# Kernel optimization log

Hardware: AMD Instinct MI355X
Metric: run time of the kernel (lower is better)

## Reference

```python
import jax, jax.numpy as jnp
import numpy as np

B, T, D = 4, 2048, 128

def setup_inputs() -> dict:
    key = jax.random.key(0)
    k1, k2, k3 = jax.random.split(key, 3)
    x = jax.random.normal(k1, (B, T, D), dtype=jnp.float32)
    # torch nn.Linear default init ~ U(-1/sqrt(D), 1/sqrt(D))
    lim = 1.0 / np.sqrt(D)
    W = jax.random.uniform(k2, (3 * D, D), dtype=jnp.float32, minval=-lim, maxval=lim)
    b = jax.random.uniform(k3, (3 * D,), dtype=jnp.float32, minval=-lim, maxval=lim)
    return {"x": x, "W": W, "b": b}

def reference(x, W, b):
    Bx, Tx, Dx = x.shape
    qkv = (x @ W.T + b).reshape(Bx, Tx, 3, Dx)
    q, k, v = qkv[:, :, 0], qkv[:, :, 1], qkv[:, :, 2]
    # positive feature map: elu(x) + 1
    q = jax.nn.elu(q) + 1.0
    k = jax.nn.elu(k) + 1.0
    # causal linear attention via outer-product cumsum (same math as torch module)
    kv = jnp.einsum('bti,btj->btij', k, v)      # (B,T,D,D)
    kv_cum = jnp.cumsum(kv, axis=1)             # prefix sums of k v^T
    k_cum = jnp.cumsum(k, axis=1)               # prefix sums of k
    num = jnp.einsum('bti,btij->btj', q, kv_cum)
    den = jnp.einsum('bti,bti->bt', q, k_cum)[..., None] + 1e-6
    return num / den
```

## Files before the change

kernel.cpp:

```cpp
#include <hip/hip_runtime.h>
#include <math.h>

#define Bn 4
#define Tn 2048
#define Dn 128
#define TDn 384
#define Cn 32
#define NCn 64
#define NCHUNK (Bn*NCn)
#define NROW (Bn*Tn)

__global__ __launch_bounds__(256) void wt_kernel(
    const float* __restrict__ W, float* __restrict__ Wt)
{
    __shared__ float t[32][33];
    const int bi = blockIdx.x >> 2;
    const int bj = blockIdx.x & 3;
    const int r0 = bi * 32, c0 = bj * 32;
    const int tr = threadIdx.x >> 5, tc = threadIdx.x & 31;
#pragma unroll
    for (int rr = tr; rr < 32; rr += 8)
        t[rr][tc] = W[(r0 + rr) * 128 + c0 + tc];
    __syncthreads();
#pragma unroll
    for (int rr = tr; rr < 32; rr += 8)
        Wt[(c0 + rr) * 384 + r0 + tc] = t[tc][rr];
}

__global__ __launch_bounds__(192) void qkv_kernel(
    const float* __restrict__ x, const float* __restrict__ Wt,
    const float* __restrict__ bias, float* __restrict__ qb,
    float* __restrict__ kb, float* __restrict__ vb)
{
    __shared__ __align__(16) float xs[16 * 128];
    const int tid = threadIdx.x;
    const int row0 = blockIdx.x * 16;

    {
        const float4* xg = (const float4*)(x + (size_t)row0 * 128);
        float4* xls = (float4*)xs;
        for (int i = tid; i < 16 * 32; i += 192) xls[i] = xg[i];
    }
    __syncthreads();

    const int c0 = tid, c1 = tid + 192;
    float acc0[16], acc1[16];
#pragma unroll
    for (int r = 0; r < 16; ++r) { acc0[r] = 0.f; acc1[r] = 0.f; }

    for (int k4 = 0; k4 < 32; ++k4) {
        float w0[4], w1[4];
#pragma unroll
        for (int u = 0; u < 4; ++u) {
            w0[u] = Wt[(size_t)(k4 * 4 + u) * 384 + c0];
            w1[u] = Wt[(size_t)(k4 * 4 + u) * 384 + c1];
        }
        float4 xv[16];
#pragma unroll
        for (int r = 0; r < 16; ++r) xv[r] = *(const float4*)&xs[r * 128 + k4 * 4];
#pragma unroll
        for (int r = 0; r < 16; ++r) {
            acc0[r] += xv[r].x * w0[0] + xv[r].y * w0[1] + xv[r].z * w0[2] + xv[r].w * w0[3];
            acc1[r] += xv[r].x * w1[0] + xv[r].y * w1[1] + xv[r].z * w1[2] + xv[r].w * w1[3];
        }
    }

    const float bb0 = bias[c0], bb1 = bias[c1];
#pragma unroll
    for (int r = 0; r < 16; ++r) {
        const size_t row = (size_t)(row0 + r);
        float v0 = acc0[r] + bb0;
        float v1 = acc1[r] + bb1;
        if (c0 < 128) qb[row * 128 + c0] = (v0 > 0.f) ? v0 + 1.f : expf(v0);
        else          kb[row * 128 + (c0 - 128)] = (v0 > 0.f) ? v0 + 1.f : expf(v0);
        if (c1 < 256) kb[row * 128 + (c1 - 128)] = (v1 > 0.f) ? v1 + 1.f : expf(v1);
        else          vb[row * 128 + (c1 - 256)] = v1;
    }
}

__global__ __launch_bounds__(256) void chunkkv_kernel(
    const float* __restrict__ kb, const float* __restrict__ vb,
    float* __restrict__ kvb, float* __restrict__ ksb)
{
    __shared__ __align__(16) float sK[32 * 132];
    __shared__ __align__(16) float sV[32 * 132];
    const int tid = threadIdx.x;
    const int cb = blockIdx.x;
    const size_t base4 = (size_t)cb * (Cn * 128 / 4);

    {
        const float4* kg = (const float4*)kb + base4;
        const float4* vg = (const float4*)vb + base4;
        for (int i4 = tid; i4 < 32 * 32; i4 += 256) {
            int r = i4 >> 5, c4 = i4 & 31;
            ((float4*)&sK[r * 132])[c4] = kg[i4];
            ((float4*)&sV[r * 132])[c4] = vg[i4];
        }
    }
    __syncthreads();

    const int ty = tid >> 4, tx = tid & 15;
    const int i0 = ty * 8, j0 = tx * 8;
    float acc[8][8];
#pragma unroll
    for (int a = 0; a < 8; ++a)
#pragma unroll
        for (int b2 = 0; b2 < 8; ++b2) acc[a][b2] = 0.f;

#pragma unroll 2
    for (int t = 0; t < 32; ++t) {
        float4 ka = *(const float4*)&sK[t * 132 + i0];
        float4 kb4 = *(const float4*)&sK[t * 132 + i0 + 4];
        float4 va = *(const float4*)&sV[t * 132 + j0];
        float4 vb4 = *(const float4*)&sV[t * 132 + j0 + 4];
        float kk[8] = {ka.x, ka.y, ka.z, ka.w, kb4.x, kb4.y, kb4.z, kb4.w};
        float vv[8] = {va.x, va.y, va.z, va.w, vb4.x, vb4.y, vb4.z, vb4.w};
#pragma unroll
        for (int a = 0; a < 8; ++a)
#pragma unroll
            for (int b2 = 0; b2 < 8; ++b2) acc[a][b2] += kk[a] * vv[b2];
    }

    float* outp = kvb + (size_t)cb * 16384;
#pragma unroll
    for (int a = 0; a < 8; ++a) {
        *(float4*)&outp[(i0 + a) * 128 + j0] =
            make_float4(acc[a][0], acc[a][1], acc[a][2], acc[a][3]);
        *(float4*)&outp[(i0 + a) * 128 + j0 + 4] =
            make_float4(acc[a][4], acc[a][5], acc[a][6], acc[a][7]);
    }

    if (tid < 128) {
        float s = 0.f;
#pragma unroll
        for (int t = 0; t < 32; ++t) s += sK[t * 132 + tid];
        ksb[cb * 128 + tid] = s;
    }
}

__global__ __launch_bounds__(256) void prefix_kernel(
    float* __restrict__ kvb, float* __restrict__ ksb)
{
    const int tid = threadIdx.x;
    if (blockIdx.x < 256) {
        const int L = blockIdx.x * 256 + tid;
        const int b = L >> 14, ij = L & 16383;
        float* p = kvb + (size_t)b * NCn * 16384 + ij;
        float run = 0.f;
        for (int g = 0; g < 4; ++g) {
            float buf[16];
#pragma unroll
            for (int j = 0; j < 16; ++j) buf[j] = p[(size_t)(g * 16 + j) * 16384];
#pragma unroll
            for (int j = 0; j < 16; ++j) {
                p[(size_t)(g * 16 + j) * 16384] = run;
                run += buf[j];
            }
        }
    } else {
        const int L = (blockIdx.x - 256) * 256 + tid;
        const int b = L >> 7, i = L & 127;
        float* p = ksb + (size_t)b * NCn * 128 + i;
        float run = 0.f;
        for (int g = 0; g < 4; ++g) {
            float buf[16];
#pragma unroll
            for (int j = 0; j < 16; ++j) buf[j] = p[(size_t)(g * 16 + j) * 128];
#pragma unroll
            for (int j = 0; j < 16; ++j) {
                p[(size_t)(g * 16 + j) * 128] = run;
                run += buf[j];
            }
        }
    }
}

__global__ __launch_bounds__(512) void out_kernel(
    const float* __restrict__ qb, const float* __restrict__ kb,
    const float* __restrict__ vb, const float* __restrict__ kvb,
    const float* __restrict__ ksb, float* __restrict__ out)
{
    __shared__ __align__(16) float sS[128 * 132];
    __shared__ __align__(16) float sQ[32 * 132];
    __shared__ __align__(16) float sK[32 * 132];
    __shared__ __align__(16) float sV[32 * 132];
    __shared__ __align__(16) float sKp[128];
    __shared__ __align__(16) float sSc[32 * 33];
    __shared__ __align__(16) float sDen[32];

    const int tid = threadIdx.x;
    const int cb = blockIdx.x;
    const size_t base4 = (size_t)cb * (Cn * 128 / 4);

    {
        const float4* gS = (const float4*)(kvb + (size_t)cb * 16384);
        for (int i4 = tid; i4 < 128 * 32; i4 += 512) {
            int r = i4 >> 5, c4 = i4 & 31;
            ((float4*)&sS[r * 132])[c4] = gS[i4];
        }
        const float4* qg = (const float4*)qb + base4;
        const float4* kg = (const float4*)kb + base4;
        const float4* vg = (const float4*)vb + base4;
        for (int i4 = tid; i4 < 32 * 32; i4 += 512) {
            int r = i4 >> 5, c4 = i4 & 31;
            ((float4*)&sQ[r * 132])[c4] = qg[i4];
            ((float4*)&sK[r * 132])[c4] = kg[i4];
            ((float4*)&sV[r * 132])[c4] = vg[i4];
        }
        if (tid < 128) sKp[tid] = ksb[cb * 128 + tid];
    }
    __syncthreads();

    for (int s = tid; s < 1024; s += 512) {
        const int t = s >> 5, tp = s & 31;
        float d = 0.f;
#pragma unroll
        for (int k4 = 0; k4 < 32; ++k4) {
            float4 a = *(const float4*)&sQ[t * 132 + k4 * 4];
            float4 b2 = *(const float4*)&sK[tp * 132 + k4 * 4];
            d += a.x * b2.x + a.y * b2.y + a.z * b2.z + a.w * b2.w;
        }
        sSc[t * 33 + tp] = (tp <= t) ? d : 0.f;
    }
    __syncthreads();

    if (tid < 32) {
        const int t = tid;
        float d = 0.f;
#pragma unroll
        for (int k4 = 0; k4 < 32; ++k4) {
            float4 a = *(const float4*)&sQ[t * 132 + k4 * 4];
            float4 b2 = *(const float4*)&sKp[k4 * 4];
            d += a.x * b2.x + a.y * b2.y + a.z * b2.z + a.w * b2.w;
        }
#pragma unroll
        for (int tp = 0; tp < 32; ++tp) d += sSc[t * 33 + tp];
        sDen[t] = d + 1e-6f;
    }

    const int ty = tid >> 4, tx = tid & 15;
    const int j0 = tx * 8;
    float acc[8];
#pragma unroll
    for (int c = 0; c < 8; ++c) acc[c] = 0.f;

    for (int i = 0; i < 128; ++i) {
        const float q0 = sQ[ty * 132 + i];
        float4 sA = *(const float4*)&sS[i * 132 + j0];
        float4 sB = *(const float4*)&sS[i * 132 + j0 + 4];
        acc[0] += q0 * sA.x; acc[1] += q0 * sA.y; acc[2] += q0 * sA.z; acc[3] += q0 * sA.w;
        acc[4] += q0 * sB.x; acc[5] += q0 * sB.y; acc[6] += q0 * sB.z; acc[7] += q0 * sB.w;
    }

#pragma unroll 2
    for (int tp = 0; tp < 32; ++tp) {
        const float s0 = sSc[ty * 33 + tp];
        float4 va = *(const float4*)&sV[tp * 132 + j0];
        float4 vb4 = *(const float4*)&sV[tp * 132 + j0 + 4];
        acc[0] += s0 * va.x; acc[1] += s0 * va.y; acc[2] += s0 * va.z; acc[3] += s0 * va.w;
        acc[4] += s0 * vb4.x; acc[5] += s0 * vb4.y; acc[6] += s0 * vb4.z; acc[7] += s0 * vb4.w;
    }
    __syncthreads();

    const float den0 = sDen[ty];
    float* o0 = out + ((size_t)cb * Cn + ty) * 128 + j0;
    *(float4*)o0 = make_float4(acc[0] / den0, acc[1] / den0, acc[2] / den0, acc[3] / den0);
    *(float4*)(o0 + 4) = make_float4(acc[4] / den0, acc[5] / den0, acc[6] / den0, acc[7] / den0);
}

extern "C" void kernel_launch(void* const* d_in, const int* in_sizes, int n_in,
                              void* d_out, int out_size, void* d_ws, size_t ws_size,
                              hipStream_t stream)
{
    const float* x = (const float*)d_in[0];
    const float* W = (const float*)d_in[1];
    const float* bias = (const float*)d_in[2];
    float* out = (float*)d_out;

    float* ws = (float*)d_ws;
    float* qb = ws;
    float* kb = ws + 1048576;
    float* vb = ws + 2097152;
    float* kvb = ws + 3145728;
    float* ksb = ws + 3145728 + 4194304;
    float* Wt  = ws + 3145728 + 4194304 + 32768;

    wt_kernel<<<48, 256, 0, stream>>>(W, Wt);
    qkv_kernel<<<NROW / 16, 192, 0, stream>>>(x, Wt, bias, qb, kb, vb);
    chunkkv_kernel<<<NCHUNK, 256, 0, stream>>>(kb, vb, kvb, ksb);
    prefix_kernel<<<258, 256, 0, stream>>>(kvb, ksb);
    out_kernel<<<NCHUNK, 512, 0, stream>>>(qb, kb, vb, kvb, ksb, out);
}
```

Before: 131.6 us.

## Fuse QKV projection, chunk KV outer product, and intra-chunk scores into one kernel

Merges the W transpose, QKV projection and per-chunk KV state kernels into a single kernel per 32-token chunk. W is transposed on the fly through shared memory, K is never written to global memory, and the masked intra-chunk score matrix and its row sums are computed here and passed to the output kernel. The output kernel drops from 512 to 256 threads, uses 4x4 register tiles, and no longer recomputes QK^T. This removes two launches and the K round trip through global memory. In exchange only 256 blocks run the projection, each reloading all of W, so the projection has less parallelism.

```diff
diff --git a/kernel.cpp b/kernel.cpp
--- a/kernel.cpp
+++ b/kernel.cpp
@@ -1,140 +1,174 @@
 #include <hip/hip_runtime.h>
 #include <math.h>
 
-#define Bn 4
-#define Tn 2048
-#define Dn 128
-#define TDn 384
-#define Cn 32
 #define NCn 64
-#define NCHUNK (Bn*NCn)
-#define NROW (Bn*Tn)
-
-__global__ __launch_bounds__(256) void wt_kernel(
-    const float* __restrict__ W, float* __restrict__ Wt)
+#define NCHUNK 256
+
+__device__ __forceinline__ float elu1(float v) {
+    return (v > 0.f) ? v + 1.f : expf(v);
+}
+
+__global__ __launch_bounds__(384) void ab_kernel(
+    const float* __restrict__ x, const float* __restrict__ W,
+    const float* __restrict__ bias,
+    float* __restrict__ qb, float* __restrict__ vb,
+    float* __restrict__ kvb, float* __restrict__ ksb,
+    float* __restrict__ scb, float* __restrict__ rsb)
 {
-    __shared__ float t[32][33];
-    const int bi = blockIdx.x >> 2;
-    const int bj = blockIdx.x & 3;
-    const int r0 = bi * 32, c0 = bj * 32;
-    const int tr = threadIdx.x >> 5, tc = threadIdx.x & 31;
-#pragma unroll
-    for (int rr = tr; rr < 32; rr += 8)
-        t[rr][tc] = W[(r0 + rr) * 128 + c0 + tc];
-    __syncthreads();
-#pragma unroll
-    for (int rr = tr; rr < 32; rr += 8)
-        Wt[(c0 + rr) * 384 + r0 + tc] = t[tc][rr];
-}
-
-__global__ __launch_bounds__(192) void qkv_kernel(
-    const float* __restrict__ x, const float* __restrict__ Wt,
-    const float* __restrict__ bias, float* __restrict__ qb,
-    float* __restrict__ kb, float* __restrict__ vb)
-{
-    __shared__ __align__(16) float xs[16 * 128];
-    const int tid = threadIdx.x;
-    const int row0 = blockIdx.x * 16;
-
-    {
-        const float4* xg = (const float4*)(x + (size_t)row0 * 128);
-        float4* xls = (float4*)xs;
-        for (int i = tid; i < 16 * 32; i += 192) xls[i] = xg[i];
-    }
-    __syncthreads();
-
-    const int c0 = tid, c1 = tid + 192;
-    float acc0[16], acc1[16];
-#pragma unroll
-    for (int r = 0; r < 16; ++r) { acc0[r] = 0.f; acc1[r] = 0.f; }
-
-    for (int k4 = 0; k4 < 32; ++k4) {
-        float w0[4], w1[4];
-#pragma unroll
-        for (int u = 0; u < 4; ++u) {
-            w0[u] = Wt[(size_t)(k4 * 4 + u) * 384 + c0];
-            w1[u] = Wt[(size_t)(k4 * 4 + u) * 384 + c1];
-        }
-        float4 xv[16];
-#pragma unroll
-        for (int r = 0; r < 16; ++r) xv[r] = *(const float4*)&xs[r * 128 + k4 * 4];
-#pragma unroll
-        for (int r = 0; r < 16; ++r) {
-            acc0[r] += xv[r].x * w0[0] + xv[r].y * w0[1] + xv[r].z * w0[2] + xv[r].w * w0[3];
-            acc1[r] += xv[r].x * w1[0] + xv[r].y * w1[1] + xv[r].z * w1[2] + xv[r].w * w1[3];
-        }
-    }
-
-    const float bb0 = bias[c0], bb1 = bias[c1];
-#pragma unroll
-    for (int r = 0; r < 16; ++r) {
-        const size_t row = (size_t)(row0 + r);
-        float v0 = acc0[r] + bb0;
-        float v1 = acc1[r] + bb1;
-        if (c0 < 128) qb[row * 128 + c0] = (v0 > 0.f) ? v0 + 1.f : expf(v0);
-        else          kb[row * 128 + (c0 - 128)] = (v0 > 0.f) ? v0 + 1.f : expf(v0);
-        if (c1 < 256) kb[row * 128 + (c1 - 128)] = (v1 > 0.f) ? v1 + 1.f : expf(v1);
-        else          vb[row * 128 + (c1 - 256)] = v1;
-    }
-}
-
-__global__ __launch_bounds__(256) void chunkkv_kernel(
-    const float* __restrict__ kb, const float* __restrict__ vb,
-    float* __restrict__ kvb, float* __restrict__ ksb)
-{
+    __shared__ __align__(16) float xs[32 * 128];
+    __shared__ __align__(16) float sWt[32 * 385];
+    __shared__ __align__(16) float sQ[32 * 132];
     __shared__ __align__(16) float sK[32 * 132];
     __shared__ __align__(16) float sV[32 * 132];
+    __shared__ __align__(16) float sSc[32 * 36];
+
     const int tid = threadIdx.x;
     const int cb = blockIdx.x;
-    const size_t base4 = (size_t)cb * (Cn * 128 / 4);
 
     {
-        const float4* kg = (const float4*)kb + base4;
-        const float4* vg = (const float4*)vb + base4;
-        for (int i4 = tid; i4 < 32 * 32; i4 += 256) {
-            int r = i4 >> 5, c4 = i4 & 31;
-            ((float4*)&sK[r * 132])[c4] = kg[i4];
-            ((float4*)&sV[r * 132])[c4] = vg[i4];
+        const float4* xg = (const float4*)(x + (size_t)cb * 4096);
+        float4* xls = (float4*)xs;
+        for (int idx = tid; idx < 1024; idx += 384) xls[idx] = xg[idx];
+    }
+
+    const int rh = tid / 192;
+    const int c0 = tid % 192;
+    const int c1 = c0 + 192;
+
+    float acc0[16], acc1[16];
+#pragma unroll
+    for (int r = 0; r < 16; ++r) { acc0[r] = 0.f; acc1[r] = 0.f; }
+
+    const float4* W4 = (const float4*)W;
+    for (int kc = 0; kc < 4; ++kc) {
+        __syncthreads();
+#pragma unroll
+        for (int p = 0; p < 8; ++p) {
+            const int flat = tid + p * 384;
+            const int c = flat >> 3, f = flat & 7;
+            float4 w = W4[c * 32 + kc * 8 + f];
+            sWt[(f * 4 + 0) * 385 + c] = w.x;
+            sWt[(f * 4 + 1) * 385 + c] = w.y;
+            sWt[(f * 4 + 2) * 385 + c] = w.z;
+            sWt[(f * 4 + 3) * 385 + c] = w.w;
+        }
+        __syncthreads();
+#pragma unroll
+        for (int k4 = 0; k4 < 8; ++k4) {
+            const float w00 = sWt[(k4*4+0)*385 + c0];
+            const float w01 = sWt[(k4*4+1)*385 + c0];
+            const float w02 = sWt[(k4*4+2)*385 + c0];
+            const float w03 = sWt[(k4*4+3)*385 + c0];
+            const float w10 = sWt[(k4*4+0)*385 + c1];
+            const float w11 = sWt[(k4*4+1)*385 + c1];
+            const float w12 = sWt[(k4*4+2)*385 + c1];
+            const float w13 = sWt[(k4*4+3)*385 + c1];
+#pragma unroll
+            for (int r = 0; r < 16; ++r) {
+                float4 xv = *(const float4*)&xs[(rh*16+r)*128 + kc*32 + k4*4];
+                acc0[r] += xv.x*w00 + xv.y*w01 + xv.z*w02 + xv.w*w03;
+                acc1[r] += xv.x*w10 + xv.y*w11 + xv.z*w12 + xv.w*w13;
+            }
+        }
+    }
+
+    {
+        const float bb0 = bias[c0], bb1 = bias[c1];
+#pragma unroll
+        for (int r = 0; r < 16; ++r) {
+            const int row = rh*16 + r;
+            float v0 = acc0[r] + bb0;
+            float v1 = acc1[r] + bb1;
+            if (c0 < 128) sQ[row*132 + c0]         = elu1(v0);
+            else          sK[row*132 + (c0 - 128)] = elu1(v0);
+            if (c1 < 256) sK[row*132 + (c1 - 128)] = elu1(v1);
+            else          sV[row*132 + (c1 - 256)] = v1;
         }
     }
     __syncthreads();
 
-    const int ty = tid >> 4, tx = tid & 15;
-    const int i0 = ty * 8, j0 = tx * 8;
-    float acc[8][8];
-#pragma unroll
-    for (int a = 0; a < 8; ++a)
-#pragma unroll
-        for (int b2 = 0; b2 < 8; ++b2) acc[a][b2] = 0.f;
-
+    {
+        float4* qg = (float4*)(qb + (size_t)cb * 4096);
+        float4* vg = (float4*)(vb + (size_t)cb * 4096);
+        for (int idx = tid; idx < 1024; idx += 384) {
+            int t = idx >> 5, c4 = idx & 31;
+            qg[idx] = *(const float4*)&sQ[t*132 + c4*4];
+            vg[idx] = *(const float4*)&sV[t*132 + c4*4];
+        }
+    }
+
+    if (tid < 256) {
+        const int i0 = (tid >> 4) * 8, j0 = (tid & 15) * 8;
+        float acc[8][8];
+#pragma unroll
+        for (int a = 0; a < 8; ++a)
+#pragma unroll
+            for (int b2 = 0; b2 < 8; ++b2) acc[a][b2] = 0.f;
 #pragma unroll 2
-    for (int t = 0; t < 32; ++t) {
-        float4 ka = *(const float4*)&sK[t * 132 + i0];
-        float4 kb4 = *(const float4*)&sK[t * 132 + i0 + 4];
-        float4 va = *(const float4*)&sV[t * 132 + j0];
-        float4 vb4 = *(const float4*)&sV[t * 132 + j0 + 4];
-        float kk[8] = {ka.x, ka.y, ka.z, ka.w, kb4.x, kb4.y, kb4.z, kb4.w};
-        float vv[8] = {va.x, va.y, va.z, va.w, vb4.x, vb4.y, vb4.z, vb4.w};
-#pragma unroll
-        for (int a = 0; a < 8; ++a)
-#pragma unroll
-            for (int b2 = 0; b2 < 8; ++b2) acc[a][b2] += kk[a] * vv[b2];
-    }
-
-    float* outp = kvb + (size_t)cb * 16384;
-#pragma unroll
-    for (int a = 0; a < 8; ++a) {
-        *(float4*)&outp[(i0 + a) * 128 + j0] =
-            make_float4(acc[a][0], acc[a][1], acc[a][2], acc[a][3]);
-        *(float4*)&outp[(i0 + a) * 128 + j0 + 4] =
-            make_float4(acc[a][4], acc[a][5], acc[a][6], acc[a][7]);
-    }
+        for (int t = 0; t < 32; ++t) {
+            float4 ka  = *(const float4*)&sK[t*132 + i0];
+            float4 kb4 = *(const float4*)&sK[t*132 + i0 + 4];
+            float4 va  = *(const float4*)&sV[t*132 + j0];
+            float4 vb4 = *(const float4*)&sV[t*132 + j0 + 4];
+            float kk[8] = {ka.x, ka.y, ka.z, ka.w, kb4.x, kb4.y, kb4.z, kb4.w};
+            float vv[8] = {va.x, va.y, va.z, va.w, vb4.x, vb4.y, vb4.z, vb4.w};
+#pragma unroll
+            for (int a = 0; a < 8; ++a)
+#pragma unroll
+                for (int b2 = 0; b2 < 8; ++b2) acc[a][b2] += kk[a] * vv[b2];
+        }
+        float* outp = kvb + (size_t)cb * 16384;
+#pragma unroll
+        for (int a = 0; a < 8; ++a) {
+            *(float4*)&outp[(i0+a)*128 + j0] =
+                make_float4(acc[a][0], acc[a][1], acc[a][2], acc[a][3]);
+            *(float4*)&outp[(i0+a)*128 + j0 + 4] =
+                make_float4(acc[a][4], acc[a][5], acc[a][6], acc[a][7]);
+        }
+    } else {
+        const int sid = tid - 256;
+        const int ta  = sid >> 3;
+        const int tp0 = (sid & 7) * 4;
+        float d0[4] = {0.f,0.f,0.f,0.f}, d1[4] = {0.f,0.f,0.f,0.f};
+#pragma unroll 4
+        for (int k4 = 0; k4 < 32; ++k4) {
+            float4 qa = *(const float4*)&sQ[ta*132 + k4*4];
+            float4 qc = *(const float4*)&sQ[(ta+16)*132 + k4*4];
+#pragma unroll
+            for (int u = 0; u < 4; ++u) {
+                float4 kv = *(const float4*)&sK[(tp0+u)*132 + k4*4];
+                d0[u] += qa.x*kv.x + qa.y*kv.y + qa.z*kv.z + qa.w*kv.w;
+                d1[u] += qc.x*kv.x + qc.y*kv.y + qc.z*kv.z + qc.w*kv.w;
+            }
+        }
+        float4 m0, m1;
+        m0.x = (tp0+0 <= ta) ? d0[0] : 0.f;
+        m0.y = (tp0+1 <= ta) ? d0[1] : 0.f;
+        m0.z = (tp0+2 <= ta) ? d0[2] : 0.f;
+        m0.w = (tp0+3 <= ta) ? d0[3] : 0.f;
+        m1.x = (tp0+0 <= ta+16) ? d1[0] : 0.f;
+        m1.y = (tp0+1 <= ta+16) ? d1[1] : 0.f;
+        m1.z = (tp0+2 <= ta+16) ? d1[2] : 0.f;
+        m1.w = (tp0+3 <= ta+16) ? d1[3] : 0.f;
+        *(float4*)&sSc[ta*36 + tp0]      = m0;
+        *(float4*)&sSc[(ta+16)*36 + tp0] = m1;
+        float4* sg = (float4*)(scb + (size_t)cb * 1024);
+        sg[ta*8 + (sid & 7)]      = m0;
+        sg[(ta+16)*8 + (sid & 7)] = m1;
+    }
+    __syncthreads();
 
     if (tid < 128) {
         float s = 0.f;
 #pragma unroll
-        for (int t = 0; t < 32; ++t) s += sK[t * 132 + tid];
-        ksb[cb * 128 + tid] = s;
+        for (int t = 0; t < 32; ++t) s += sK[t*132 + tid];
+        ksb[cb*128 + tid] = s;
+    } else if (tid < 160) {
+        const int t = tid - 128;
+        float s = 0.f;
+#pragma unroll
+        for (int tp = 0; tp < 32; ++tp) s += sSc[t*36 + tp];
+        rsb[cb*32 + t] = s;
     }
 }
 
@@ -150,10 +184,10 @@
         for (int g = 0; g < 4; ++g) {
             float buf[16];
 #pragma unroll
-            for (int j = 0; j < 16; ++j) buf[j] = p[(size_t)(g * 16 + j) * 16384];
+            for (int j = 0; j < 16; ++j) buf[j] = p[(size_t)(g*16 + j) * 16384];
 #pragma unroll
             for (int j = 0; j < 16; ++j) {
-                p[(size_t)(g * 16 + j) * 16384] = run;
+                p[(size_t)(g*16 + j) * 16384] = run;
                 run += buf[j];
             }
         }
@@ -165,129 +199,140 @@
         for (int g = 0; g < 4; ++g) {
             float buf[16];
 #pragma unroll
-            for (int j = 0; j < 16; ++j) buf[j] = p[(size_t)(g * 16 + j) * 128];
+            for (int j = 0; j < 16; ++j) buf[j] = p[(size_t)(g*16 + j) * 128];
 #pragma unroll
             for (int j = 0; j < 16; ++j) {
-                p[(size_t)(g * 16 + j) * 128] = run;
+                p[(size_t)(g*16 + j) * 128] = run;
                 run += buf[j];
             }
         }
     }
 }
 
-__global__ __launch_bounds__(512) void out_kernel(
-    const float* __restrict__ qb, const float* __restrict__ kb,
-    const float* __restrict__ vb, const float* __restrict__ kvb,
-    const float* __restrict__ ksb, float* __restrict__ out)
+__global__ __launch_bounds__(256) void out_kernel(
+    const float* __restrict__ qb, const float* __restrict__ vb,
+    const float* __restrict__ kvb, const float* __restrict__ ksb,
+    const float* __restrict__ scb, const float* __restrict__ rsb,
+    float* __restrict__ out)
 {
-    __shared__ __align__(16) float sS[128 * 132];
+    __shared__ __align__(16) float sS[128 * 128];
     __shared__ __align__(16) float sQ[32 * 132];
-    __shared__ __align__(16) float sK[32 * 132];
     __shared__ __align__(16) float sV[32 * 132];
+    __shared__ __align__(16) float sSc[32 * 36];
     __shared__ __align__(16) float sKp[128];
-    __shared__ __align__(16) float sSc[32 * 33];
-    __shared__ __align__(16) float sDen[32];
+    __shared__ float sDen[32];
 
     const int tid = threadIdx.x;
     const int cb = blockIdx.x;
-    const size_t base4 = (size_t)cb * (Cn * 128 / 4);
 
     {
         const float4* gS = (const float4*)(kvb + (size_t)cb * 16384);
-        for (int i4 = tid; i4 < 128 * 32; i4 += 512) {
-            int r = i4 >> 5, c4 = i4 & 31;
-            ((float4*)&sS[r * 132])[c4] = gS[i4];
-        }
-        const float4* qg = (const float4*)qb + base4;
-        const float4* kg = (const float4*)kb + base4;
-        const float4* vg = (const float4*)vb + base4;
-        for (int i4 = tid; i4 < 32 * 32; i4 += 512) {
-            int r = i4 >> 5, c4 = i4 & 31;
-            ((float4*)&sQ[r * 132])[c4] = qg[i4];
-            ((float4*)&sK[r * 132])[c4] = kg[i4];
-            ((float4*)&sV[r * 132])[c4] = vg[i4];
-        }
-        if (tid < 128) sKp[tid] = ksb[cb * 128 + tid];
+        float4* sS4 = (float4*)sS;
+#pragma unroll
+        for (int j = 0; j < 16; ++j) sS4[tid + j*256] = gS[tid + j*256];
+        const float4* qg = (const float4*)(qb + (size_t)cb * 4096);
+        const float4* vg = (const float4*)(vb + (size_t)cb * 4096);
+#pragma unroll
+        for (int j = 0; j < 4; ++j) {
+            int idx = tid + j*256;
+            int t = idx >> 5, c4 = idx & 31;
+            *(float4*)&sQ[t*132 + c4*4] = qg[idx];
+            *(float4*)&sV[t*132 + c4*4] = vg[idx];
+        }
+        const float4* sg = (const float4*)(scb + (size_t)cb * 1024);
+        int t = tid >> 3, p4 = tid & 7;
+        *(float4*)&sSc[t*36 + p4*4] = sg[tid];
+        if (tid < 128) sKp[tid] = ksb[cb*128 + tid];
     }
     __syncthreads();
 
-    for (int s = tid; s < 1024; s += 512) {
-        const int t = s >> 5, tp = s & 31;
+    if (tid < 32) {
         float d = 0.f;
 #pragma unroll
         for (int k4 = 0; k4 < 32; ++k4) {
-            float4 a = *(const float4*)&sQ[t * 132 + k4 * 4];
-            float4 b2 = *(const float4*)&sK[tp * 132 + k4 * 4];
-            d += a.x * b2.x + a.y * b2.y + a.z * b2.z + a.w * b2.w;
-        }
-        sSc[t * 33 + tp] = (tp <= t) ? d : 0.f;
+            float4 a  = *(const float4*)&sQ[tid*132 + k4*4];
+            float4 b2 = *(const float4*)&sKp[k4*4];
+            d += a.x*b2.x + a.y*b2.y + a.z*b2.z + a.w*b2.w;
+        }
+        sDen[tid] = d + rsb[cb*32 + tid] + 1e-6f;
+    }
+
+    const int r0 = (tid >> 5) * 4;
+    const int c0 = (tid & 31) * 4;
+    float acc[4][4];
+#pragma unroll
+    for (int a = 0; a < 4; ++a)
+#pragma unroll
+        for (int b2 = 0; b2 < 4; ++b2) acc[a][b2] = 0.f;
+
+    for (int k4 = 0; k4 < 32; ++k4) {
+        float qr[4][4];
+#pragma unroll
+        for (int rr = 0; rr < 4; ++rr) {
+            float4 t4 = *(const float4*)&sQ[(r0+rr)*132 + k4*4];
+            qr[rr][0]=t4.x; qr[rr][1]=t4.y; qr[rr][2]=t4.z; qr[rr][3]=t4.w;
+        }
+#pragma unroll
+        for (int u = 0; u < 4; ++u) {
+            float4 s4 = *(const float4*)&sS[(k4*4+u)*128 + c0];
+#pragma unroll
+            for (int rr = 0; rr < 4; ++rr) {
+                acc[rr][0] += qr[rr][u]*s4.x;
+                acc[rr][1] += qr[rr][u]*s4.y;
+                acc[rr][2] += qr[rr][u]*s4.z;
+                acc[rr][3] += qr[rr][u]*s4.w;
+            }
+        }
+    }
+
+#pragma unroll
+    for (int p4 = 0; p4 < 8; ++p4) {
+        float sr[4][4];
+#pragma unroll
+        for (int rr = 0; rr < 4; ++rr) {
+            float4 t4 = *(const float4*)&sSc[(r0+rr)*36 + p4*4];
+            sr[rr][0]=t4.x; sr[rr][1]=t4.y; sr[rr][2]=t4.z; sr[rr][3]=t4.w;
+        }
+#pragma unroll
+        for (int u = 0; u < 4; ++u) {
+            float4 v4 = *(const float4*)&sV[(p4*4+u)*132 + c0];
+#pragma unroll
+            for (int rr = 0; rr < 4; ++rr) {
+                acc[rr][0] += sr[rr][u]*v4.x;
+                acc[rr][1] += sr[rr][u]*v4.y;
+                acc[rr][2] += sr[rr][u]*v4.z;
+                acc[rr][3] += sr[rr][u]*v4.w;
+            }
+        }
     }
     __syncthreads();
 
-    if (tid < 32) {
-        const int t = tid;
-        float d = 0.f;
-#pragma unroll
-        for (int k4 = 0; k4 < 32; ++k4) {
-            float4 a = *(const float4*)&sQ[t * 132 + k4 * 4];
-            float4 b2 = *(const float4*)&sKp[k4 * 4];
-            d += a.x * b2.x + a.y * b2.y + a.z * b2.z + a.w * b2.w;
-        }
-#pragma unroll
-        for (int tp = 0; tp < 32; ++tp) d += sSc[t * 33 + tp];
-        sDen[t] = d + 1e-6f;
-    }
-
-    const int ty = tid >> 4, tx = tid & 15;
-    const int j0 = tx * 8;
-    float acc[8];
-#pragma unroll
-    for (int c = 0; c < 8; ++c) acc[c] = 0.f;
-
-    for (int i = 0; i < 128; ++i) {
-        const float q0 = sQ[ty * 132 + i];
-        float4 sA = *(const float4*)&sS[i * 132 + j0];
-        float4 sB = *(const float4*)&sS[i * 132 + j0 + 4];
-        acc[0] += q0 * sA.x; acc[1] += q0 * sA.y; acc[2] += q0 * sA.z; acc[3] += q0 * sA.w;
-        acc[4] += q0 * sB.x; acc[5] += q0 * sB.y; acc[6] += q0 * sB.z; acc[7] += q0 * sB.w;
-    }
-
-#pragma unroll 2
-    for (int tp = 0; tp < 32; ++tp) {
-        const float s0 = sSc[ty * 33 + tp];
-        float4 va = *(const float4*)&sV[tp * 132 + j0];
-        float4 vb4 = *(const float4*)&sV[tp * 132 + j0 + 4];
-        acc[0] += s0 * va.x; acc[1] += s0 * va.y; acc[2] += s0 * va.z; acc[3] += s0 * va.w;
-        acc[4] += s0 * vb4.x; acc[5] += s0 * vb4.y; acc[6] += s0 * vb4.z; acc[7] += s0 * vb4.w;
-    }
-    __syncthreads();
-
-    const float den0 = sDen[ty];
-    float* o0 = out + ((size_t)cb * Cn + ty) * 128 + j0;
-    *(float4*)o0 = make_float4(acc[0] / den0, acc[1] / den0, acc[2] / den0, acc[3] / den0);
-    *(float4*)(o0 + 4) = make_float4(acc[4] / den0, acc[5] / den0, acc[6] / den0, acc[7] / den0);
+#pragma unroll
+    for (int rr = 0; rr < 4; ++rr) {
+        const float dv = sDen[r0+rr];
+        *(float4*)(out + ((size_t)cb*32 + r0+rr)*128 + c0) =
+            make_float4(acc[rr][0]/dv, acc[rr][1]/dv, acc[rr][2]/dv, acc[rr][3]/dv);
+    }
 }
 
 extern "C" void kernel_launch(void* const* d_in, const int* in_sizes, int n_in,
                               void* d_out, int out_size, void* d_ws, size_t ws_size,
                               hipStream_t stream)
 {
-    const float* x = (const float*)d_in[0];
-    const float* W = (const float*)d_in[1];
+    const float* x    = (const float*)d_in[0];
+    const float* W    = (const float*)d_in[1];
     const float* bias = (const float*)d_in[2];
     float* out = (float*)d_out;
 
-    float* ws = (float*)d_ws;
-    float* qb = ws;
-    float* kb = ws + 1048576;
-    float* vb = ws + 2097152;
-    float* kvb = ws + 3145728;
-    float* ksb = ws + 3145728 + 4194304;
-    float* Wt  = ws + 3145728 + 4194304 + 32768;
-
-    wt_kernel<<<48, 256, 0, stream>>>(W, Wt);
-    qkv_kernel<<<NROW / 16, 192, 0, stream>>>(x, Wt, bias, qb, kb, vb);
-    chunkkv_kernel<<<NCHUNK, 256, 0, stream>>>(kb, vb, kvb, ksb);
+    float* ws  = (float*)d_ws;
+    float* qb  = ws;
+    float* vb  = ws + 1048576;
+    float* kvb = ws + 2097152;
+    float* ksb = ws + 6291456;
+    float* scb = ws + 6324224;
+    float* rsb = ws + 6586368;
+
+    ab_kernel<<<NCHUNK, 384, 0, stream>>>(x, W, bias, qb, vb, kvb, ksb, scb, rsb);
     prefix_kernel<<<258, 256, 0, stream>>>(kvb, ksb);
-    out_kernel<<<NCHUNK, 512, 0, stream>>>(qb, kb, vb, kvb, ksb, out);
-}
+    out_kernel<<<NCHUNK, 256, 0, stream>>>(qb, vb, kvb, ksb, scb, rsb, out);
+}
```

New measurement: 210.2 us. 1.6x slower.

## Split chunk-state and output kernels across more blocks; precompute intra-chunk scores

Applied to the files above, without the earlier changes.

Chunk KV-state computation is split into two column halves per chunk, giving twice as many blocks. The intra-chunk causal QK^T scores and their row sums move into the same kernel as extra blocks, written to workspace. The output kernel is split four ways along the value dimension, reading the prefix state directly from global memory instead of staging the whole 128x128 state in shared memory. This raises parallelism and occupancy at the cost of extra workspace traffic and redundant Q loads per block.

```diff
diff --git a/kernel.cpp b/kernel.cpp
--- a/kernel.cpp
+++ b/kernel.cpp
@@ -1,14 +1,13 @@
 #include <hip/hip_runtime.h>
 #include <math.h>
 
-#define Bn 4
-#define Tn 2048
-#define Dn 128
-#define TDn 384
-#define Cn 32
 #define NCn 64
-#define NCHUNK (Bn*NCn)
-#define NROW (Bn*Tn)
+#define NCHUNK 256
+#define NROW 8192
+
+__device__ __forceinline__ float elu1(float v) {
+    return (v > 0.f) ? v + 1.f : expf(v);
+}
 
 __global__ __launch_bounds__(256) void wt_kernel(
     const float* __restrict__ W, float* __restrict__ Wt)
@@ -71,70 +70,123 @@
         const size_t row = (size_t)(row0 + r);
         float v0 = acc0[r] + bb0;
         float v1 = acc1[r] + bb1;
-        if (c0 < 128) qb[row * 128 + c0] = (v0 > 0.f) ? v0 + 1.f : expf(v0);
-        else          kb[row * 128 + (c0 - 128)] = (v0 > 0.f) ? v0 + 1.f : expf(v0);
-        if (c1 < 256) kb[row * 128 + (c1 - 128)] = (v1 > 0.f) ? v1 + 1.f : expf(v1);
+        if (c0 < 128) qb[row * 128 + c0] = elu1(v0);
+        else          kb[row * 128 + (c0 - 128)] = elu1(v0);
+        if (c1 < 256) kb[row * 128 + (c1 - 128)] = elu1(v1);
         else          vb[row * 128 + (c1 - 256)] = v1;
     }
 }
 
-__global__ __launch_bounds__(256) void chunkkv_kernel(
-    const float* __restrict__ kb, const float* __restrict__ vb,
-    float* __restrict__ kvb, float* __restrict__ ksb)
-{
-    __shared__ __align__(16) float sK[32 * 132];
-    __shared__ __align__(16) float sV[32 * 132];
+__global__ __launch_bounds__(256) void cs_kernel(
+    const float* __restrict__ qb, const float* __restrict__ kb,
+    const float* __restrict__ vb,
+    float* __restrict__ kvb, float* __restrict__ ksb,
+    float* __restrict__ scb, float* __restrict__ rsb)
+{
+    __shared__ __align__(16) float smem[9600];
     const int tid = threadIdx.x;
-    const int cb = blockIdx.x;
-    const size_t base4 = (size_t)cb * (Cn * 128 / 4);
-
-    {
-        const float4* kg = (const float4*)kb + base4;
-        const float4* vg = (const float4*)vb + base4;
-        for (int i4 = tid; i4 < 32 * 32; i4 += 256) {
-            int r = i4 >> 5, c4 = i4 & 31;
-            ((float4*)&sK[r * 132])[c4] = kg[i4];
-            ((float4*)&sV[r * 132])[c4] = vg[i4];
-        }
-    }
-    __syncthreads();
-
-    const int ty = tid >> 4, tx = tid & 15;
-    const int i0 = ty * 8, j0 = tx * 8;
-    float acc[8][8];
-#pragma unroll
-    for (int a = 0; a < 8; ++a)
-#pragma unroll
-        for (int b2 = 0; b2 < 8; ++b2) acc[a][b2] = 0.f;
+    const int b = blockIdx.x;
+
+    if (b < 512) {
+        const int cb = b >> 1, jh = b & 1;
+        float* sK  = smem;
+        float* sVh = smem + 4224;
+        {
+            const float4* kg = (const float4*)(kb + (size_t)cb * 4096);
+#pragma unroll
+            for (int i = 0; i < 4; ++i) {
+                int idx = tid + i * 256;
+                int r = idx >> 5, c4 = idx & 31;
+                *(float4*)&sK[r * 132 + c4 * 4] = kg[idx];
+            }
+            const float* vg = vb + (size_t)cb * 4096 + jh * 64;
+#pragma unroll
+            for (int i = 0; i < 2; ++i) {
+                int idx = tid + i * 256;
+                int r = idx >> 4, c4 = idx & 15;
+                *(float4*)&sVh[r * 68 + c4 * 4] = *(const float4*)(vg + r * 128 + c4 * 4);
+            }
+        }
+        __syncthreads();
+
+        const int i0 = (tid >> 4) * 8;
+        const int j0 = (tid & 15) * 4;
+        float acc[8][4];
+#pragma unroll
+        for (int a = 0; a < 8; ++a)
+#pragma unroll
+            for (int c = 0; c < 4; ++c) acc[a][c] = 0.f;
 
 #pragma unroll 2
-    for (int t = 0; t < 32; ++t) {
-        float4 ka = *(const float4*)&sK[t * 132 + i0];
-        float4 kb4 = *(const float4*)&sK[t * 132 + i0 + 4];
-        float4 va = *(const float4*)&sV[t * 132 + j0];
-        float4 vb4 = *(const float4*)&sV[t * 132 + j0 + 4];
-        float kk[8] = {ka.x, ka.y, ka.z, ka.w, kb4.x, kb4.y, kb4.z, kb4.w};
-        float vv[8] = {va.x, va.y, va.z, va.w, vb4.x, vb4.y, vb4.z, vb4.w};
+        for (int t = 0; t < 32; ++t) {
+            float4 ka  = *(const float4*)&sK[t * 132 + i0];
+            float4 kb4 = *(const float4*)&sK[t * 132 + i0 + 4];
+            float4 vv  = *(const float4*)&sVh[t * 68 + j0];
+            float kk[8] = {ka.x, ka.y, ka.z, ka.w, kb4.x, kb4.y, kb4.z, kb4.w};
+#pragma unroll
+            for (int a = 0; a < 8; ++a) {
+                acc[a][0] += kk[a] * vv.x;
+                acc[a][1] += kk[a] * vv.y;
+                acc[a][2] += kk[a] * vv.z;
+                acc[a][3] += kk[a] * vv.w;
+            }
+        }
+        float* outp = kvb + (size_t)cb * 16384 + jh * 64;
 #pragma unroll
         for (int a = 0; a < 8; ++a)
-#pragma unroll
-            for (int b2 = 0; b2 < 8; ++b2) acc[a][b2] += kk[a] * vv[b2];
-    }
-
-    float* outp = kvb + (size_t)cb * 16384;
-#pragma unroll
-    for (int a = 0; a < 8; ++a) {
-        *(float4*)&outp[(i0 + a) * 128 + j0] =
-            make_float4(acc[a][0], acc[a][1], acc[a][2], acc[a][3]);
-        *(float4*)&outp[(i0 + a) * 128 + j0 + 4] =
-            make_float4(acc[a][4], acc[a][5], acc[a][6], acc[a][7]);
-    }
-
-    if (tid < 128) {
-        float s = 0.f;
-#pragma unroll
-        for (int t = 0; t < 32; ++t) s += sK[t * 132 + tid];
-        ksb[cb * 128 + tid] = s;
+            *(float4*)&outp[(i0 + a) * 128 + j0] =
+                make_float4(acc[a][0], acc[a][1], acc[a][2], acc[a][3]);
+    } else {
+        const int cb = b - 512;
+        float* sQ  = smem;
+        float* sK2 = smem + 4224;
+        float* sSc = smem + 8448;
+        {
+            const float4* qg = (const float4*)(qb + (size_t)cb * 4096);
+            const float4* kg = (const float4*)(kb + (size_t)cb * 4096);
+#pragma unroll
+            for (int i = 0; i < 4; ++i) {
+                int idx = tid + i * 256;
+                int r = idx >> 5, c4 = idx & 31;
+                *(float4*)&sQ[r * 132 + c4 * 4]  = qg[idx];
+                *(float4*)&sK2[r * 132 + c4 * 4] = kg[idx];
+            }
+        }
+        __syncthreads();
+
+        const int ta  = tid >> 3;
+        const int tp0 = (tid & 7) * 4;
+        float d[4] = {0.f, 0.f, 0.f, 0.f};
+#pragma unroll 4
+        for (int k4 = 0; k4 < 32; ++k4) {
+            float4 qa = *(const float4*)&sQ[ta * 132 + k4 * 4];
+#pragma unroll
+            for (int u = 0; u < 4; ++u) {
+                float4 kv = *(const float4*)&sK2[(tp0 + u) * 132 + k4 * 4];
+                d[u] += qa.x * kv.x + qa.y * kv.y + qa.z * kv.z + qa.w * kv.w;
+            }
+        }
+        float4 m;
+        m.x = (tp0 + 0 <= ta) ? d[0] : 0.f;
+        m.y = (tp0 + 1 <= ta) ? d[1] : 0.f;
+        m.z = (tp0 + 2 <= ta) ? d[2] : 0.f;
+        m.w = (tp0 + 3 <= ta) ? d[3] : 0.f;
+        *(float4*)&sSc[ta * 36 + tp0] = m;
+        *(float4*)(scb + (size_t)cb * 1024 + ta * 32 + tp0) = m;
+        __syncthreads();
+
+        if (tid < 32) {
+            float s = 0.f;
+#pragma unroll
+            for (int tp = 0; tp < 32; ++tp) s += sSc[tid * 36 + tp];
+            rsb[cb * 32 + tid] = s;
+        } else if (tid >= 64 && tid < 192) {
+            const int i = tid - 64;
+            float s = 0.f;
+#pragma unroll
+            for (int t = 0; t < 32; ++t) s += sK2[t * 132 + i];
+            ksb[cb * 128 + i] = s;
+        }
     }
 }
 
@@ -175,119 +227,98 @@
     }
 }
 
-__global__ __launch_bounds__(512) void out_kernel(
-    const float* __restrict__ qb, const float* __restrict__ kb,
-    const float* __restrict__ vb, const float* __restrict__ kvb,
-    const float* __restrict__ ksb, float* __restrict__ out)
-{
-    __shared__ __align__(16) float sS[128 * 132];
+__global__ __launch_bounds__(256) void out_kernel(
+    const float* __restrict__ qb, const float* __restrict__ vb,
+    const float* __restrict__ kvb, const float* __restrict__ ksb,
+    const float* __restrict__ scb, const float* __restrict__ rsb,
+    float* __restrict__ out)
+{
     __shared__ __align__(16) float sQ[32 * 132];
-    __shared__ __align__(16) float sK[32 * 132];
-    __shared__ __align__(16) float sV[32 * 132];
+    __shared__ __align__(16) float sVs[32 * 36];
+    __shared__ __align__(16) float sSc[32 * 36];
     __shared__ __align__(16) float sKp[128];
-    __shared__ __align__(16) float sSc[32 * 33];
-    __shared__ __align__(16) float sDen[32];
+    __shared__ float sDen[32];
 
     const int tid = threadIdx.x;
-    const int cb = blockIdx.x;
-    const size_t base4 = (size_t)cb * (Cn * 128 / 4);
+    const int cb = blockIdx.x >> 2;
+    const int ch = blockIdx.x & 3;
 
     {
-        const float4* gS = (const float4*)(kvb + (size_t)cb * 16384);
-        for (int i4 = tid; i4 < 128 * 32; i4 += 512) {
-            int r = i4 >> 5, c4 = i4 & 31;
-            ((float4*)&sS[r * 132])[c4] = gS[i4];
-        }
-        const float4* qg = (const float4*)qb + base4;
-        const float4* kg = (const float4*)kb + base4;
-        const float4* vg = (const float4*)vb + base4;
-        for (int i4 = tid; i4 < 32 * 32; i4 += 512) {
-            int r = i4 >> 5, c4 = i4 & 31;
-            ((float4*)&sQ[r * 132])[c4] = qg[i4];
-            ((float4*)&sK[r * 132])[c4] = kg[i4];
-            ((float4*)&sV[r * 132])[c4] = vg[i4];
+        const float4* qg = (const float4*)(qb + (size_t)cb * 4096);
+#pragma unroll
+        for (int i = 0; i < 4; ++i) {
+            int idx = tid + i * 256;
+            int r = idx >> 5, c4 = idx & 31;
+            *(float4*)&sQ[r * 132 + c4 * 4] = qg[idx];
+        }
+        {
+            int r = tid >> 3, c4 = tid & 7;
+            *(float4*)&sVs[r * 36 + c4 * 4] =
+                *(const float4*)(vb + (size_t)cb * 4096 + r * 128 + ch * 32 + c4 * 4);
+            *(float4*)&sSc[r * 36 + c4 * 4] =
+                *(const float4*)(scb + (size_t)cb * 1024 + tid * 4);
         }
         if (tid < 128) sKp[tid] = ksb[cb * 128 + tid];
     }
     __syncthreads();
 
-    for (int s = tid; s < 1024; s += 512) {
-        const int t = s >> 5, tp = s & 31;
+    if (tid < 32) {
         float d = 0.f;
 #pragma unroll
         for (int k4 = 0; k4 < 32; ++k4) {
-            float4 a = *(const float4*)&sQ[t * 132 + k4 * 4];
-            float4 b2 = *(const float4*)&sK[tp * 132 + k4 * 4];
-            d += a.x * b2.x + a.y * b2.y + a.z * b2.z + a.w * b2.w;
-        }
-        sSc[t * 33 + tp] = (tp <= t) ? d : 0.f;
-    }
-    __syncthreads();
-
-    if (tid < 32) {
-        const int t = tid;
-        float d = 0.f;
-#pragma unroll
-        for (int k4 = 0; k4 < 32; ++k4) {
-            float4 a = *(const float4*)&sQ[t * 132 + k4 * 4];
+            float4 a  = *(const float4*)&sQ[tid * 132 + k4 * 4];
             float4 b2 = *(const float4*)&sKp[k4 * 4];
             d += a.x * b2.x + a.y * b2.y + a.z * b2.z + a.w * b2.w;
         }
-#pragma unroll
-        for (int tp = 0; tp < 32; ++tp) d += sSc[t * 33 + tp];
-        sDen[t] = d + 1e-6f;
-    }
-
-    const int ty = tid >> 4, tx = tid & 15;
-    const int j0 = tx * 8;
-    float acc[8];
-#pragma unroll
-    for (int c = 0; c < 8; ++c) acc[c] = 0.f;
-
-    for (int i = 0; i < 128; ++i) {
-        const float q0 = sQ[ty * 132 + i];
-        float4 sA = *(const float4*)&sS[i * 132 + j0];
-        float4 sB = *(const float4*)&sS[i * 132 + j0 + 4];
-        acc[0] += q0 * sA.x; acc[1] += q0 * sA.y; acc[2] += q0 * sA.z; acc[3] += q0 * sA.w;
-        acc[4] += q0 * sB.x; acc[5] += q0 * sB.y; acc[6] += q0 * sB.z; acc[7] += q0 * sB.w;
-    }
-
-#pragma unroll 2
+        sDen[tid] = d + rsb[cb * 32 + tid] + 1e-6f;
+    }
+
+    const int row = tid >> 3;
+    const int c4  = tid & 7;
+    const float* Sg = kvb + (size_t)cb * 16384 + ch * 32 + c4 * 4;
+
+    float a0 = 0.f, a1 = 0.f, a2 = 0.f, a3 = 0.f;
+#pragma unroll 8
+    for (int k = 0; k < 128; ++k) {
+        const float qv = sQ[row * 132 + k];
+        float4 s = *(const float4*)(Sg + (size_t)k * 128);
+        a0 += qv * s.x; a1 += qv * s.y; a2 += qv * s.z; a3 += qv * s.w;
+    }
+#pragma unroll 8
     for (int tp = 0; tp < 32; ++tp) {
-        const float s0 = sSc[ty * 33 + tp];
-        float4 va = *(const float4*)&sV[tp * 132 + j0];
-        float4 vb4 = *(const float4*)&sV[tp * 132 + j0 + 4];
-        acc[0] += s0 * va.x; acc[1] += s0 * va.y; acc[2] += s0 * va.z; acc[3] += s0 * va.w;
-        acc[4] += s0 * vb4.x; acc[5] += s0 * vb4.y; acc[6] += s0 * vb4.z; acc[7] += s0 * vb4.w;
+        const float sc = sSc[row * 36 + tp];
+        float4 v = *(const float4*)&sVs[tp * 36 + c4 * 4];
+        a0 += sc * v.x; a1 += sc * v.y; a2 += sc * v.z; a3 += sc * v.w;
     }
     __syncthreads();
 
-    const float den0 = sDen[ty];
-    float* o0 = out + ((size_t)cb * Cn + ty) * 128 + j0;
-    *(float4*)o0 = make_float4(acc[0] / den0, acc[1] / den0, acc[2] / den0, acc[3] / den0);
-    *(float4*)(o0 + 4) = make_float4(acc[4] / den0, acc[5] / den0, acc[6] / den0, acc[7] / den0);
+    const float dv = sDen[row];
+    *(float4*)(out + ((size_t)cb * 32 + row) * 128 + ch * 32 + c4 * 4) =
+        make_float4(a0 / dv, a1 / dv, a2 / dv, a3 / dv);
 }
 
 extern "C" void kernel_launch(void* const* d_in, const int* in_sizes, int n_in,
                               void* d_out, int out_size, void* d_ws, size_t ws_size,
                               hipStream_t stream)
 {
-    const float* x = (const float*)d_in[0];
-    const float* W = (const float*)d_in[1];
+    const float* x    = (const float*)d_in[0];
+    const float* W    = (const float*)d_in[1];
     const float* bias = (const float*)d_in[2];
     float* out = (float*)d_out;
 
-    float* ws = (float*)d_ws;
-    float* qb = ws;
-    float* kb = ws + 1048576;
-    float* vb = ws + 2097152;
+    float* ws  = (float*)d_ws;
+    float* qb  = ws;
+    float* kb  = ws + 1048576;
+    float* vb  = ws + 2097152;
     float* kvb = ws + 3145728;
-    float* ksb = ws + 3145728 + 4194304;
-    float* Wt  = ws + 3145728 + 4194304 + 32768;
+    float* ksb = ws + 7340032;
+    float* scb = ws + 7372800;
+    float* rsb = ws + 7634944;
+    float* Wt  = ws + 7643136;
 
     wt_kernel<<<48, 256, 0, stream>>>(W, Wt);
     qkv_kernel<<<NROW / 16, 192, 0, stream>>>(x, Wt, bias, qb, kb, vb);
-    chunkkv_kernel<<<NCHUNK, 256, 0, stream>>>(kb, vb, kvb, ksb);
+    cs_kernel<<<768, 256, 0, stream>>>(qb, kb, vb, kvb, ksb, scb, rsb);
     prefix_kernel<<<258, 256, 0, stream>>>(kvb, ksb);
-    out_kernel<<<NCHUNK, 512, 0, stream>>>(qb, kb, vb, kvb, ksb, out);
-}
+    out_kernel<<<1024, 256, 0, stream>>>(qb, vb, kvb, ksb, scb, rsb, out);
+}
```

Measured after the change: 133.3 us. No clear change (+1.3%).
